# Performance work log

Hardware: AMD Instinct MI355X
Metric: run time of the kernel (lower is better)

The kernel has to match this reference:

```python
import jax, jax.numpy as jnp
import numpy as np

B, L, D = 16, 1024, 256
H, FF = 8, 2048
DH = D // H
EPS = 1e-5


def setup_inputs() -> dict:
    key = jax.random.key(0)
    ks = jax.random.split(key, 13)
    s = 0.02
    return {
        "x": jax.random.normal(ks[0], (B, L, D), jnp.float32),
        "Wq": jax.random.normal(ks[1], (D, D), jnp.float32) * s,
        "bq": jnp.zeros((D,), jnp.float32),
        "Wk": jax.random.normal(ks[2], (D, D), jnp.float32) * s,
        "bk": jnp.zeros((D,), jnp.float32),
        "Wv": jax.random.normal(ks[3], (D, D), jnp.float32) * s,
        "bv": jnp.zeros((D,), jnp.float32),
        "Wo": jax.random.normal(ks[4], (D, D), jnp.float32) * s,
        "bo": jnp.zeros((D,), jnp.float32),
        "W1": jax.random.normal(ks[5], (D, FF), jnp.float32) * s,
        "b1": jnp.zeros((FF,), jnp.float32),
        "W2": jax.random.normal(ks[6], (FF, D), jnp.float32) * s,
        "b2": jnp.zeros((D,), jnp.float32),
        "g1": jnp.ones((D,), jnp.float32),
        "be1": jnp.zeros((D,), jnp.float32),
        "g2": jnp.ones((D,), jnp.float32),
        "be2": jnp.zeros((D,), jnp.float32),
    }


def _layernorm(x, g, b):
    m = jnp.mean(x, axis=-1, keepdims=True)
    v = jnp.mean(jnp.square(x - m), axis=-1, keepdims=True)
    return (x - m) * jax.lax.rsqrt(v + EPS) * g + b


def reference(x, Wq, bq, Wk, bk, Wv, bv, Wo, bo, W1, b1, W2, b2, g1, be1, g2, be2):
    b, l, d = x.shape
    # QKV projections, split heads (torch split/cat == reshape to [b,l,H,dh])
    q = (x @ Wq + bq).reshape(b, l, H, DH)
    k = (x @ Wk + bk).reshape(b, l, H, DH)
    v = (x @ Wv + bv).reshape(b, l, H, DH)
    # scaled dot-product attention per head
    scores = jnp.einsum("bqhd,bkhd->bhqk", q, k) / np.float32(DH) ** 0.5
    attn = jax.nn.softmax(scores, axis=-1)
    o = jnp.einsum("bhqk,bkhd->bqhd", attn, v).reshape(b, l, d)
    o = o @ Wo + bo
    # residual + LN1 (dropout p=0.0 -> identity)
    h = _layernorm(x + o, g1, be1)
    # FFN + residual + LN2
    ff = jax.nn.relu(h @ W1 + b1) @ W2 + b2
    return _layernorm(h + ff, g2, be2)
```

## Files before the change

kernel.cpp:

```cpp
#include <hip/hip_runtime.h>
#include <math.h>

#define B_  16
#define L_  1024
#define D_  256
#define H_  8
#define DH_ 32
#define FF_ 2048
#define NROW (B_*L_)
#define QKVS 768

typedef __attribute__((ext_vector_type(8))) short short8;
typedef __attribute__((ext_vector_type(4))) short short4v;
typedef __attribute__((ext_vector_type(4))) float f32x4;
typedef __attribute__((ext_vector_type(4))) unsigned uint4v;
typedef __attribute__((ext_vector_type(4))) unsigned short ushort4v;
typedef unsigned short ushortT;

__device__ inline ushortT f2bf(float f) {
    unsigned u = __builtin_bit_cast(unsigned, f);
    u += 0x7fffu + ((u >> 16) & 1u);
    return (ushortT)(u >> 16);
}

__device__ inline float bf2f(ushortT u) {
    return __builtin_bit_cast(float, (unsigned)u << 16);
}

__device__ inline float fexp2(float x) {
#if __has_builtin(__builtin_amdgcn_exp2f)
    return __builtin_amdgcn_exp2f(x);
#else
    return exp2f(x);
#endif
}

__device__ inline void gload_lds16(const ushortT* g, ushortT* l) {
    __builtin_amdgcn_global_load_lds(
        (const __attribute__((address_space(1))) unsigned*)g,
        (__attribute__((address_space(3))) unsigned*)l, 16, 0, 0);
}

__device__ inline unsigned lds_addr(const void* p) {
    return (unsigned)(size_t)(const __attribute__((address_space(3))) void*)p;
}

template<bool RELU, bool OBF16>
__global__ __launch_bounds__(256)
void gemm_bf16_kernel(const ushortT* __restrict__ A, const ushortT* __restrict__ Bt,
                      const float* __restrict__ bias, void* __restrict__ Cv,
                      int K, int ldb, int ldc)
{
    __shared__ ushortT As[2][128 * 32];
    __shared__ ushortT Bs[2][128 * 32];

    const int tid   = threadIdx.x;
    const int w     = tid >> 6;
    const int lane  = tid & 63;
    const int qlane = lane & 15;
    const int g     = lane >> 4;
    const int wm    = w >> 1, wn = w & 1;
    const int m0    = (blockIdx.x & 127) * 128;
    const int n0    = (blockIdx.x >> 7) * 128;

    int srowA[2], sq[2];
    #pragma unroll
    for (int j = 0; j < 2; ++j) {
        int idx = (j * 4 + w) * 64 + lane;
        srowA[j] = idx >> 2;
        sq[j]    = (idx & 3) ^ (srowA[j] & 3);
    }
    const int rsw = (g ^ (qlane & 3)) * 8;

    f32x4 acc[4][4];
    #pragma unroll
    for (int mi = 0; mi < 4; ++mi)
        #pragma unroll
        for (int ni = 0; ni < 4; ++ni)
            acc[mi][ni] = (f32x4){0.f, 0.f, 0.f, 0.f};

    auto stage = [&](int buf, int kt) {
        const int k0 = kt * 32;
        #pragma unroll
        for (int j = 0; j < 2; ++j) {
            gload_lds16(A + (size_t)(m0 + srowA[j]) * K + k0 + sq[j] * 8,
                        &As[buf][(j * 4 + w) * 512]);
            gload_lds16(Bt + (size_t)(n0 + srowA[j]) * ldb + k0 + sq[j] * 8,
                        &Bs[buf][(j * 4 + w) * 512]);
        }
    };

    stage(0, 0);
    __syncthreads();

    const int nt = K >> 5;
    for (int t = 0; t < nt; ++t) {
        const int cur = t & 1;
        if (t + 1 < nt) stage(cur ^ 1, t + 1);

        short8 af[4], bfr[4];
        #pragma unroll
        for (int mi = 0; mi < 4; ++mi)
            af[mi] = *(const short8*)&As[cur][(wm * 64 + mi * 16 + qlane) * 32 + rsw];
        #pragma unroll
        for (int ni = 0; ni < 4; ++ni)
            bfr[ni] = *(const short8*)&Bs[cur][(wn * 64 + ni * 16 + qlane) * 32 + rsw];

        #pragma unroll
        for (int mi = 0; mi < 4; ++mi)
            #pragma unroll
            for (int ni = 0; ni < 4; ++ni)
                acc[mi][ni] = __builtin_amdgcn_mfma_f32_16x16x32_bf16(
                    af[mi], bfr[ni], acc[mi][ni], 0, 0, 0);

        __syncthreads();
    }

    #pragma unroll
    for (int mi = 0; mi < 4; ++mi) {
        #pragma unroll
        for (int ni = 0; ni < 4; ++ni) {
            const int n = n0 + wn * 64 + ni * 16 + qlane;
            const float bval = bias ? bias[n] : 0.f;
            #pragma unroll
            for (int r = 0; r < 4; ++r) {
                const int m = m0 + wm * 64 + mi * 16 + 4 * g + r;
                float v = acc[mi][ni][r] + bval;
                if (RELU)  v = fmaxf(v, 0.f);
                if (OBF16) ((ushortT*)Cv)[(size_t)m * ldc + n] = f2bf(v);
                else       ((float*)Cv)[(size_t)m * ldc + n] = v;
            }
        }
    }
}

template<bool RELU, bool OBF16>
__global__ __launch_bounds__(256)
void gemm64_kernel(const ushortT* __restrict__ A, const ushortT* __restrict__ Bt,
                   const float* __restrict__ bias, void* __restrict__ Cv,
                   int K, int ldc)
{
    __shared__ ushortT As[2][64 * 64];
    __shared__ ushortT Bs[2][64 * 64];

    const int tid   = threadIdx.x;
    const int w     = tid >> 6;
    const int lane  = tid & 63;
    const int qlane = lane & 15;
    const int g     = lane >> 4;
    const int bid   = blockIdx.x;
    const int m0    = (bid & 255) * 64;
    const int n0    = (bid >> 8) * 64;

    int srow[2], sq[2];
    #pragma unroll
    for (int j = 0; j < 2; ++j) {
        const int c = j * 256 + tid;
        srow[j] = c >> 3;
        sq[j]   = (c & 7) ^ (srow[j] & 7);
    }

    f32x4 acc[4];
    #pragma unroll
    for (int ni = 0; ni < 4; ++ni) acc[ni] = (f32x4){0.f, 0.f, 0.f, 0.f};

    auto stage = [&](int buf, int kt) {
        const int k0 = kt * 64;
        #pragma unroll
        for (int j = 0; j < 2; ++j) {
            gload_lds16(A + (size_t)(m0 + srow[j]) * K + k0 + sq[j] * 8,
                        &As[buf][(j * 256 + tid) * 8]);
            gload_lds16(Bt + (size_t)(n0 + srow[j]) * K + k0 + sq[j] * 8,
                        &Bs[buf][(j * 256 + tid) * 8]);
        }
    };

    stage(0, 0);
    __syncthreads();

    const int arow = w * 16 + qlane;
    const int nt = K >> 6;
    for (int t = 0; t < nt; ++t) {
        const int cur = t & 1;
        if (t + 1 < nt) stage(cur ^ 1, t + 1);

        #pragma unroll
        for (int ks = 0; ks < 2; ++ks) {
            const int aq = (ks * 4 + g) ^ (arow & 7);
            short8 af = *(const short8*)&As[cur][arow * 64 + aq * 8];
            #pragma unroll
            for (int ni = 0; ni < 4; ++ni) {
                const int brow = ni * 16 + qlane;
                const int bq = (ks * 4 + g) ^ (brow & 7);
                short8 bfr = *(const short8*)&Bs[cur][brow * 64 + bq * 8];
                acc[ni] = __builtin_amdgcn_mfma_f32_16x16x32_bf16(af, bfr, acc[ni], 0, 0, 0);
            }
        }

        __syncthreads();
    }

    #pragma unroll
    for (int ni = 0; ni < 4; ++ni) {
        const int n = n0 + ni * 16 + qlane;
        const float bval = bias[n];
        #pragma unroll
        for (int r = 0; r < 4; ++r) {
            const int m = m0 + w * 16 + 4 * g + r;
            float v = acc[ni][r] + bval;
            if (RELU)  v = fmaxf(v, 0.f);
            if (OBF16) ((ushortT*)Cv)[(size_t)m * ldc + n] = f2bf(v);
            else       ((float*)Cv)[(size_t)m * ldc + n] = v;
        }
    }
}

template<bool XF32, bool YF32, bool OBF16>
__global__ __launch_bounds__(256)
void ln_kernel(const void* __restrict__ X, const void* __restrict__ Y,
               const float* __restrict__ g, const float* __restrict__ bb,
               void* __restrict__ out)
{
    const int tid  = threadIdx.x;
    const int lane = tid & 63;
    const int w    = tid >> 6;
    const size_t row = (size_t)blockIdx.x * 4 + w;
    const int c    = lane * 4;

    float xv[4], yv[4];
    if (XF32) {
        float4 v = *reinterpret_cast<const float4*>((const float*)X + row * D_ + c);
        xv[0] = v.x; xv[1] = v.y; xv[2] = v.z; xv[3] = v.w;
    } else {
        ushort4v v = *reinterpret_cast<const ushort4v*>((const ushortT*)X + row * D_ + c);
        #pragma unroll
        for (int j = 0; j < 4; ++j) xv[j] = bf2f(v[j]);
    }
    if (YF32) {
        float4 v = *reinterpret_cast<const float4*>((const float*)Y + row * D_ + c);
        yv[0] = v.x; yv[1] = v.y; yv[2] = v.z; yv[3] = v.w;
    } else {
        ushort4v v = *reinterpret_cast<const ushort4v*>((const ushortT*)Y + row * D_ + c);
        #pragma unroll
        for (int j = 0; j < 4; ++j) yv[j] = bf2f(v[j]);
    }

    float s0 = xv[0] + yv[0], s1 = xv[1] + yv[1], s2 = xv[2] + yv[2], s3 = xv[3] + yv[3];

    float sum = s0 + s1 + s2 + s3;
    float sq  = s0 * s0 + s1 * s1 + s2 * s2 + s3 * s3;
    #pragma unroll
    for (int off = 1; off < 64; off <<= 1) {
        sum += __shfl_xor(sum, off);
        sq  += __shfl_xor(sq, off);
    }
    const float mean = sum * (1.f / D_);
    const float var  = sq * (1.f / D_) - mean * mean;
    const float rinv = rsqrtf(var + 1e-5f);

    const float4 gv = *reinterpret_cast<const float4*>(g + c);
    const float4 bv = *reinterpret_cast<const float4*>(bb + c);
    float o0 = (s0 - mean) * rinv * gv.x + bv.x;
    float o1 = (s1 - mean) * rinv * gv.y + bv.y;
    float o2 = (s2 - mean) * rinv * gv.z + bv.z;
    float o3 = (s3 - mean) * rinv * gv.w + bv.w;

    if (OBF16) {
        unsigned p0 = (unsigned)f2bf(o0) | ((unsigned)f2bf(o1) << 16);
        unsigned p1 = (unsigned)f2bf(o2) | ((unsigned)f2bf(o3) << 16);
        uint2 u = {p0, p1};
        *reinterpret_cast<uint2*>((ushortT*)out + row * D_ + c) = u;
    } else {
        float4 ov = {o0, o1, o2, o3};
        *reinterpret_cast<float4*>((float*)out + row * D_ + c) = ov;
    }
}

__global__ __launch_bounds__(512)
void attn_mfma_kernel(const ushortT* __restrict__ qkv, ushortT* __restrict__ o)
{
    __shared__ __align__(16) ushortT K4[2][2][2048];
    __shared__ __align__(16) ushortT Vs[2][2][2048];

    const int tid   = threadIdx.x;
    const int lane  = tid & 63;
    const int w     = tid >> 6;
    const int qlane = lane & 15;
    const int g     = lane >> 4;

    const int bid = blockIdx.x;
    const int bh  = bid & 127;
    const int b   = bh >> 3;
    const int h   = bh & 7;
    const int q0  = (bid >> 7) * 128;

    const size_t inbase = (size_t)b * L_ * QKVS + h * 32;
    const size_t obase  = (size_t)b * L_ * 256 + h * 32;

    const short8 qf = *(const short8*)(qkv + inbase + (size_t)(q0 + w * 16 + qlane) * QKVS + g * 8);

    f32x4 ot0 = {0.f, 0.f, 0.f, 0.f}, ot1 = {0.f, 0.f, 0.f, 0.f};
    float l_reg = 0.f;

    const float CEXP = 0.25503540f;

    const int t2   = tid & 255;
    const int skey = t2 >> 2;
    const int sg   = t2 & 3;
    const bool isK = tid < 256;
    const ushortT* src = qkv + inbase + (isK ? 256 : 512) + sg * 8 + (size_t)skey * QKVS;

    char* K4b = (char*)&K4[0][0][0];
    char* Vsb = (char*)&Vs[0][0][0];

    unsigned kwoff = (unsigned)sg * 1024u + (unsigned)skey * 16u;
    kwoff ^= (kwoff >> 5) & 0x60;
    const unsigned vwoff = ((unsigned)((skey >> 2) * 2 + (sg >> 1))) * 128u +
                           ((unsigned)(skey & 3)) * 32u +
                           ((((unsigned)(sg & 1)) ^ ((unsigned)(sg >> 1))) * 16u);
    char* wbase = isK ? K4b : Vsb;
    const unsigned woff = isK ? kwoff : vwoff;

    unsigned kroff[4];
    #pragma unroll
    for (int kt4 = 0; kt4 < 4; ++kt4) {
        unsigned off = (unsigned)g * 1024u + (unsigned)(kt4 * 16 + qlane) * 16u;
        kroff[kt4] = off ^ ((off >> 5) & 0x60);
    }
    const unsigned vrbase  = lds_addr(&Vs[0][0][0]) + 256u * (unsigned)g + 8u * (unsigned)qlane;
    const unsigned vrbase2 = vrbase ^ 64u;

    short8 reg0 = *(const short8*)src;
    short8 reg1 = *(const short8*)(src + (size_t)64 * QKVS);

    for (int t = 0; t < L_ / 128; ++t) {
        const unsigned bo = (unsigned)(t & 1) * 8192u;
        *(short8*)(wbase + bo + woff)         = reg0;
        *(short8*)(wbase + bo + 4096u + woff) = reg1;
        if (t + 1 < L_ / 128) {
            const size_t roff = (size_t)((t + 1) * 128) * QKVS;
            reg0 = *(const short8*)(src + roff);
            reg1 = *(const short8*)(src + roff + (size_t)64 * QKVS);
        }
        __syncthreads();

        #pragma unroll
        for (int sub = 0; sub < 2; ++sub) {
            const unsigned so = bo + (unsigned)sub * 4096u;

            f32x4 st[4];
            __builtin_amdgcn_s_setprio(1);
            #pragma unroll
            for (int kt4 = 0; kt4 < 4; ++kt4) {
                short8 kf = *(const short8*)(K4b + so + kroff[kt4]);
                st[kt4] = __builtin_amdgcn_mfma_f32_16x16x32_bf16(kf, qf, (f32x4){0.f,0.f,0.f,0.f}, 0, 0, 0);
            }
            __builtin_amdgcn_s_setprio(0);

            float p[16];
            float s4[4];
            #pragma unroll
            for (int kt4 = 0; kt4 < 4; ++kt4) {
                #pragma unroll
                for (int r = 0; r < 4; ++r)
                    p[kt4 * 4 + r] = fexp2(st[kt4][r] * CEXP);
                s4[kt4] = (p[kt4*4] + p[kt4*4+1]) + (p[kt4*4+2] + p[kt4*4+3]);
            }
            float ssum = (s4[0] + s4[1]) + (s4[2] + s4[3]);
            ssum += __shfl_xor(ssum, 16);
            ssum += __shfl_xor(ssum, 32);
            l_reg += ssum;

            unsigned pk_[8];
            #pragma unroll
            for (int i = 0; i < 8; ++i)
                asm("v_cvt_pk_bf16_f32 %0, %1, %2" : "=v"(pk_[i]) : "v"(p[2*i]), "v"(p[2*i+1]));
            const short8 pa0 = __builtin_bit_cast(short8, (uint4v){pk_[0], pk_[1], pk_[2], pk_[3]});
            const short8 pa1 = __builtin_bit_cast(short8, (uint4v){pk_[4], pk_[5], pk_[6], pk_[7]});

            const unsigned va  = vrbase  + so;
            const unsigned va2 = vrbase2 + so;
            __builtin_amdgcn_s_setprio(1);
            {
                short4v v00, v01, v10, v11;
                asm volatile("ds_read_b64_tr_b16 %0, %1"             : "=v"(v00) : "v"(va));
                asm volatile("ds_read_b64_tr_b16 %0, %1 offset:1024" : "=v"(v01) : "v"(va));
                asm volatile("ds_read_b64_tr_b16 %0, %1 offset:128"  : "=v"(v10) : "v"(va2));
                asm volatile("ds_read_b64_tr_b16 %0, %1 offset:1152" : "=v"(v11) : "v"(va2));
                asm volatile("s_waitcnt lgkmcnt(0)" ::: "memory");
                __builtin_amdgcn_sched_barrier(0);
                short8 vb0 = __builtin_shufflevector(v00, v01, 0,1,2,3,4,5,6,7);
                short8 vb1 = __builtin_shufflevector(v10, v11, 0,1,2,3,4,5,6,7);
                ot0 = __builtin_amdgcn_mfma_f32_16x16x32_bf16(pa0, vb0, ot0, 0, 0, 0);
                ot1 = __builtin_amdgcn_mfma_f32_16x16x32_bf16(pa0, vb1, ot1, 0, 0, 0);
            }
            {
                short4v v00, v01, v10, v11;
                asm volatile("ds_read_b64_tr_b16 %0, %1 offset:2048" : "=v"(v00) : "v"(va));
                asm volatile("ds_read_b64_tr_b16 %0, %1 offset:3072" : "=v"(v01) : "v"(va));
                asm volatile("ds_read_b64_tr_b16 %0, %1 offset:2176" : "=v"(v10) : "v"(va2));
                asm volatile("ds_read_b64_tr_b16 %0, %1 offset:3200" : "=v"(v11) : "v"(va2));
                asm volatile("s_waitcnt lgkmcnt(0)" ::: "memory");
                __builtin_amdgcn_sched_barrier(0);
                short8 vb0 = __builtin_shufflevector(v00, v01, 0,1,2,3,4,5,6,7);
                short8 vb1 = __builtin_shufflevector(v10, v11, 0,1,2,3,4,5,6,7);
                ot0 = __builtin_amdgcn_mfma_f32_16x16x32_bf16(pa1, vb0, ot0, 0, 0, 0);
                ot1 = __builtin_amdgcn_mfma_f32_16x16x32_bf16(pa1, vb1, ot1, 0, 0, 0);
            }
            __builtin_amdgcn_s_setprio(0);
        }
    }

    const float linv = 1.f / l_reg;
    #pragma unroll
    for (int r = 0; r < 4; ++r) {
        float lr = __shfl(linv, 4 * g + r);
        size_t row = (size_t)(q0 + w * 16 + 4 * g + r);
        ushortT* op = o + obase + row * 256;
        op[qlane]      = f2bf(ot0[r] * lr);
        op[16 + qlane] = f2bf(ot1[r] * lr);
    }
}

__global__ __launch_bounds__(256)
void prep_kernel(const float* __restrict__ x, ushortT* __restrict__ xb,
                 const float* __restrict__ Wq, const float* __restrict__ Wk,
                 const float* __restrict__ Wv, const float* __restrict__ Wo,
                 ushortT* __restrict__ Wqkvb, ushortT* __restrict__ Wob,
                 const float* __restrict__ W1, ushortT* __restrict__ W1b,
                 const float* __restrict__ W2, ushortT* __restrict__ W2b,
                 const float* __restrict__ bq, const float* __restrict__ bk,
                 const float* __restrict__ bv, float* __restrict__ bqkv)
{
    __shared__ float t[32][33];
    const int bid = blockIdx.x;
    const int tid = threadIdx.x;

    if (bid < 4096) {
        const int i = (bid * 256 + tid) * 4;
        float4 v = *reinterpret_cast<const float4*>(x + i);
        unsigned p0 = (unsigned)f2bf(v.x) | ((unsigned)f2bf(v.y) << 16);
        unsigned p1 = (unsigned)f2bf(v.z) | ((unsigned)f2bf(v.w) << 16);
        uint2 u = {p0, p1};
        *reinterpret_cast<uint2*>(xb + i) = u;
        return;
    }
    int i = bid - 4096;
    const float* W; ushortT* Wt; int K, N, bx, by;
    if (i < 256) {
        const int which = i >> 6, j = i & 63;
        bx = j & 7; by = j >> 3; K = 256; N = 256;
        W  = which == 0 ? Wq : which == 1 ? Wk : which == 2 ? Wv : Wo;
        Wt = which == 0 ? Wqkvb : which == 1 ? Wqkvb + 65536
           : which == 2 ? Wqkvb + 131072 : Wob;
    } else if (i < 768) {
        const int j = i - 256; bx = j & 63; by = j >> 6; K = 256; N = 2048;
        W = W1; Wt = W1b;
    } else if (i < 1280) {
        const int j = i - 768; bx = j & 7; by = j >> 3; K = 2048; N = 256;
        W = W2; Wt = W2b;
    } else {
        for (int k = tid; k < 768; k += 256)
            bqkv[k] = k < 256 ? bq[k] : (k < 512 ? bk[k - 256] : bv[k - 512]);
        return;
    }
    const int tx = tid & 31, ty = tid >> 5;
    const int k0 = by * 32, n0 = bx * 32;
    #pragma unroll
    for (int r = ty; r < 32; r += 8) t[r][tx] = W[(size_t)(k0 + r) * N + n0 + tx];
    __syncthreads();
    #pragma unroll
    for (int r = ty; r < 32; r += 8) Wt[(size_t)(n0 + r) * K + k0 + tx] = f2bf(t[tx][r]);
}

extern "C" void kernel_launch(void* const* d_in, const int* in_sizes, int n_in,
                              void* d_out, int out_size, void* d_ws, size_t ws_size,
                              hipStream_t stream)
{
    const float* x   = (const float*)d_in[0];
    const float* Wq  = (const float*)d_in[1];
    const float* bq  = (const float*)d_in[2];
    const float* Wk  = (const float*)d_in[3];
    const float* bk  = (const float*)d_in[4];
    const float* Wv  = (const float*)d_in[5];
    const float* bv  = (const float*)d_in[6];
    const float* Wo  = (const float*)d_in[7];
    const float* bo  = (const float*)d_in[8];
    const float* W1  = (const float*)d_in[9];
    const float* b1  = (const float*)d_in[10];
    const float* W2  = (const float*)d_in[11];
    const float* b2  = (const float*)d_in[12];
    const float* g1  = (const float*)d_in[13];
    const float* be1 = (const float*)d_in[14];
    const float* g2  = (const float*)d_in[15];
    const float* be2 = (const float*)d_in[16];
    float* out = (float*)d_out;

    char* wsb = (char*)d_ws;
    const size_t MB = (size_t)1 << 20;
    ushortT* Wqkvb = (ushortT*)(wsb);
    ushortT* Wob   = (ushortT*)(wsb + 393216);
    ushortT* W1b   = (ushortT*)(wsb + 512 * 1024);
    ushortT* W2b   = (ushortT*)(wsb + 1536 * 1024);
    float*   bqkv  = (float*)  (wsb + 2560 * 1024);
    ushortT* xb  = (ushortT*)(wsb + 3 * MB);
    ushortT* qkv = (ushortT*)(wsb + 11 * MB);
    ushortT* ob  = (ushortT*)(wsb + 35 * MB);
    ushortT* ao  = (ushortT*)(wsb + 43 * MB);
    ushortT* hb  = (ushortT*)(wsb + 3 * MB);
    ushortT* f1  = (ushortT*)(wsb + 11 * MB);

    prep_kernel<<<dim3(5377), dim3(256), 0, stream>>>(
        x, xb, Wq, Wk, Wv, Wo, Wqkvb, Wob, W1, W1b, W2, W2b, bq, bk, bv, bqkv);

    gemm_bf16_kernel<false, true><<<dim3(768), dim3(256), 0, stream>>>(
        xb, Wqkvb, bqkv, qkv, 256, 256, QKVS);

    attn_mfma_kernel<<<dim3(1024), dim3(512), 0, stream>>>(qkv, ob);

    gemm64_kernel<false, true><<<dim3(1024), dim3(256), 0, stream>>>(
        ob, Wob, bo, ao, 256, 256);

    ln_kernel<false, false, true><<<dim3(NROW / 4), dim3(256), 0, stream>>>(
        xb, ao, g1, be1, hb);

    gemm64_kernel<true, true><<<dim3(8192), dim3(256), 0, stream>>>(
        hb, W1b, b1, f1, 256, FF_);

    gemm64_kernel<false, false><<<dim3(1024), dim3(256), 0, stream>>>(
        f1, W2b, b2, out, 2048, 256);

    ln_kernel<false, true, false><<<dim3(NROW / 4), dim3(256), 0, stream>>>(
        hb, out, g2, be2, out);
}
```

Baseline: 137.9 us.

## Pack FFN1 outputs with permuted columns and shrink attention K/V tile

The FFN1 GEMM epilogue now writes four bias-added, ReLU'd bf16 values per lane as one packed 8-byte store, using hardware bf16 pack conversion. The columns of the intermediate activation are permuted to make this possible, and the prep kernel permutes W2's K dimension to match so the FFN2 result is unchanged. This replaces scalar 2-byte scattered stores on the largest intermediate tensor. Separately, the attention kernel stages 64 keys per iteration instead of 128, halving shared memory, which may raise occupancy at the cost of twice as many barriers.

```diff
diff --git a/kernel.cpp b/kernel.cpp
--- a/kernel.cpp
+++ b/kernel.cpp
@@ -134,7 +134,7 @@
     }
 }
 
-template<bool RELU, bool OBF16>
+template<bool RELU, bool OBF16, bool PACKPERM>
 __global__ __launch_bounds__(256)
 void gemm64_kernel(const ushortT* __restrict__ A, const ushortT* __restrict__ Bt,
                    const float* __restrict__ bias, void* __restrict__ Cv,
@@ -200,17 +200,38 @@
         __syncthreads();
     }
 
-    #pragma unroll
-    for (int ni = 0; ni < 4; ++ni) {
-        const int n = n0 + ni * 16 + qlane;
-        const float bval = bias[n];
+    if (PACKPERM) {
+        float bval[4];
+        #pragma unroll
+        for (int ni = 0; ni < 4; ++ni) bval[ni] = bias[n0 + ni * 16 + qlane];
         #pragma unroll
         for (int r = 0; r < 4; ++r) {
             const int m = m0 + w * 16 + 4 * g + r;
-            float v = acc[ni][r] + bval;
-            if (RELU)  v = fmaxf(v, 0.f);
-            if (OBF16) ((ushortT*)Cv)[(size_t)m * ldc + n] = f2bf(v);
-            else       ((float*)Cv)[(size_t)m * ldc + n] = v;
+            float v0 = acc[0][r] + bval[0], v1 = acc[1][r] + bval[1];
+            float v2 = acc[2][r] + bval[2], v3 = acc[3][r] + bval[3];
+            if (RELU) {
+                v0 = fmaxf(v0, 0.f); v1 = fmaxf(v1, 0.f);
+                v2 = fmaxf(v2, 0.f); v3 = fmaxf(v3, 0.f);
+            }
+            unsigned lo, hi;
+            asm("v_cvt_pk_bf16_f32 %0, %1, %2" : "=v"(lo) : "v"(v0), "v"(v1));
+            asm("v_cvt_pk_bf16_f32 %0, %1, %2" : "=v"(hi) : "v"(v2), "v"(v3));
+            uint2 u = {lo, hi};
+            *reinterpret_cast<uint2*>(&((ushortT*)Cv)[(size_t)m * ldc + n0 + qlane * 4]) = u;
+        }
+    } else {
+        #pragma unroll
+        for (int ni = 0; ni < 4; ++ni) {
+            const int n = n0 + ni * 16 + qlane;
+            const float bval = bias[n];
+            #pragma unroll
+            for (int r = 0; r < 4; ++r) {
+                const int m = m0 + w * 16 + 4 * g + r;
+                float v = acc[ni][r] + bval;
+                if (RELU)  v = fmaxf(v, 0.f);
+                if (OBF16) ((ushortT*)Cv)[(size_t)m * ldc + n] = f2bf(v);
+                else       ((float*)Cv)[(size_t)m * ldc + n] = v;
+            }
         }
     }
 }
@@ -279,8 +300,8 @@
 __global__ __launch_bounds__(512)
 void attn_mfma_kernel(const ushortT* __restrict__ qkv, ushortT* __restrict__ o)
 {
-    __shared__ __align__(16) ushortT K4[2][2][2048];
-    __shared__ __align__(16) ushortT Vs[2][2][2048];
+    __shared__ __align__(16) ushortT K4[2][2048];
+    __shared__ __align__(16) ushortT Vs[2][2048];
 
     const int tid   = threadIdx.x;
     const int lane  = tid & 63;
@@ -310,8 +331,8 @@
     const bool isK = tid < 256;
     const ushortT* src = qkv + inbase + (isK ? 256 : 512) + sg * 8 + (size_t)skey * QKVS;
 
-    char* K4b = (char*)&K4[0][0][0];
-    char* Vsb = (char*)&Vs[0][0][0];
+    char* K4b = (char*)&K4[0][0];
+    char* Vsb = (char*)&Vs[0][0];
 
     unsigned kwoff = (unsigned)sg * 1024u + (unsigned)skey * 16u;
     kwoff ^= (kwoff >> 5) & 0x60;
@@ -327,88 +348,79 @@
         unsigned off = (unsigned)g * 1024u + (unsigned)(kt4 * 16 + qlane) * 16u;
         kroff[kt4] = off ^ ((off >> 5) & 0x60);
     }
-    const unsigned vrbase  = lds_addr(&Vs[0][0][0]) + 256u * (unsigned)g + 8u * (unsigned)qlane;
+    const unsigned vrbase  = lds_addr(&Vs[0][0]) + 256u * (unsigned)g + 8u * (unsigned)qlane;
     const unsigned vrbase2 = vrbase ^ 64u;
 
-    short8 reg0 = *(const short8*)src;
-    short8 reg1 = *(const short8*)(src + (size_t)64 * QKVS);
-
-    for (int t = 0; t < L_ / 128; ++t) {
-        const unsigned bo = (unsigned)(t & 1) * 8192u;
-        *(short8*)(wbase + bo + woff)         = reg0;
-        *(short8*)(wbase + bo + 4096u + woff) = reg1;
-        if (t + 1 < L_ / 128) {
-            const size_t roff = (size_t)((t + 1) * 128) * QKVS;
-            reg0 = *(const short8*)(src + roff);
-            reg1 = *(const short8*)(src + roff + (size_t)64 * QKVS);
-        }
+    short8 reg = *(const short8*)src;
+
+    #pragma unroll 2
+    for (int t = 0; t < L_ / 64; ++t) {
+        const unsigned bo = (unsigned)(t & 1) * 4096u;
+        *(short8*)(wbase + bo + woff) = reg;
+        if (t + 1 < L_ / 64)
+            reg = *(const short8*)(src + (size_t)((t + 1) * 64) * QKVS);
         __syncthreads();
 
-        #pragma unroll
-        for (int sub = 0; sub < 2; ++sub) {
-            const unsigned so = bo + (unsigned)sub * 4096u;
-
-            f32x4 st[4];
-            __builtin_amdgcn_s_setprio(1);
+        f32x4 st[4];
+        __builtin_amdgcn_s_setprio(1);
+        #pragma unroll
+        for (int kt4 = 0; kt4 < 4; ++kt4) {
+            short8 kf = *(const short8*)(K4b + bo + kroff[kt4]);
+            st[kt4] = __builtin_amdgcn_mfma_f32_16x16x32_bf16(kf, qf, (f32x4){0.f,0.f,0.f,0.f}, 0, 0, 0);
+        }
+        __builtin_amdgcn_s_setprio(0);
+
+        float p[16];
+        float s4[4];
+        #pragma unroll
+        for (int kt4 = 0; kt4 < 4; ++kt4) {
             #pragma unroll
-            for (int kt4 = 0; kt4 < 4; ++kt4) {
-                short8 kf = *(const short8*)(K4b + so + kroff[kt4]);
-                st[kt4] = __builtin_amdgcn_mfma_f32_16x16x32_bf16(kf, qf, (f32x4){0.f,0.f,0.f,0.f}, 0, 0, 0);
-            }
-            __builtin_amdgcn_s_setprio(0);
-
-            float p[16];
-            float s4[4];
-            #pragma unroll
-            for (int kt4 = 0; kt4 < 4; ++kt4) {
-                #pragma unroll
-                for (int r = 0; r < 4; ++r)
-                    p[kt4 * 4 + r] = fexp2(st[kt4][r] * CEXP);
-                s4[kt4] = (p[kt4*4] + p[kt4*4+1]) + (p[kt4*4+2] + p[kt4*4+3]);
-            }
-            float ssum = (s4[0] + s4[1]) + (s4[2] + s4[3]);
-            ssum += __shfl_xor(ssum, 16);
-            ssum += __shfl_xor(ssum, 32);
-            l_reg += ssum;
-
-            unsigned pk_[8];
-            #pragma unroll
-            for (int i = 0; i < 8; ++i)
-                asm("v_cvt_pk_bf16_f32 %0, %1, %2" : "=v"(pk_[i]) : "v"(p[2*i]), "v"(p[2*i+1]));
-            const short8 pa0 = __builtin_bit_cast(short8, (uint4v){pk_[0], pk_[1], pk_[2], pk_[3]});
-            const short8 pa1 = __builtin_bit_cast(short8, (uint4v){pk_[4], pk_[5], pk_[6], pk_[7]});
-
-            const unsigned va  = vrbase  + so;
-            const unsigned va2 = vrbase2 + so;
-            __builtin_amdgcn_s_setprio(1);
-            {
-                short4v v00, v01, v10, v11;
-                asm volatile("ds_read_b64_tr_b16 %0, %1"             : "=v"(v00) : "v"(va));
-                asm volatile("ds_read_b64_tr_b16 %0, %1 offset:1024" : "=v"(v01) : "v"(va));
-                asm volatile("ds_read_b64_tr_b16 %0, %1 offset:128"  : "=v"(v10) : "v"(va2));
-                asm volatile("ds_read_b64_tr_b16 %0, %1 offset:1152" : "=v"(v11) : "v"(va2));
-                asm volatile("s_waitcnt lgkmcnt(0)" ::: "memory");
-                __builtin_amdgcn_sched_barrier(0);
-                short8 vb0 = __builtin_shufflevector(v00, v01, 0,1,2,3,4,5,6,7);
-                short8 vb1 = __builtin_shufflevector(v10, v11, 0,1,2,3,4,5,6,7);
-                ot0 = __builtin_amdgcn_mfma_f32_16x16x32_bf16(pa0, vb0, ot0, 0, 0, 0);
-                ot1 = __builtin_amdgcn_mfma_f32_16x16x32_bf16(pa0, vb1, ot1, 0, 0, 0);
-            }
-            {
-                short4v v00, v01, v10, v11;
-                asm volatile("ds_read_b64_tr_b16 %0, %1 offset:2048" : "=v"(v00) : "v"(va));
-                asm volatile("ds_read_b64_tr_b16 %0, %1 offset:3072" : "=v"(v01) : "v"(va));
-                asm volatile("ds_read_b64_tr_b16 %0, %1 offset:2176" : "=v"(v10) : "v"(va2));
-                asm volatile("ds_read_b64_tr_b16 %0, %1 offset:3200" : "=v"(v11) : "v"(va2));
-                asm volatile("s_waitcnt lgkmcnt(0)" ::: "memory");
-                __builtin_amdgcn_sched_barrier(0);
-                short8 vb0 = __builtin_shufflevector(v00, v01, 0,1,2,3,4,5,6,7);
-                short8 vb1 = __builtin_shufflevector(v10, v11, 0,1,2,3,4,5,6,7);
-                ot0 = __builtin_amdgcn_mfma_f32_16x16x32_bf16(pa1, vb0, ot0, 0, 0, 0);
-                ot1 = __builtin_amdgcn_mfma_f32_16x16x32_bf16(pa1, vb1, ot1, 0, 0, 0);
-            }
-            __builtin_amdgcn_s_setprio(0);
-        }
+            for (int r = 0; r < 4; ++r)
+                p[kt4 * 4 + r] = fexp2(st[kt4][r] * CEXP);
+            s4[kt4] = (p[kt4*4] + p[kt4*4+1]) + (p[kt4*4+2] + p[kt4*4+3]);
+        }
+        float ssum = (s4[0] + s4[1]) + (s4[2] + s4[3]);
+        ssum += __shfl_xor(ssum, 16);
+        ssum += __shfl_xor(ssum, 32);
+        l_reg += ssum;
+
+        unsigned pk_[8];
+        #pragma unroll
+        for (int i = 0; i < 8; ++i)
+            asm("v_cvt_pk_bf16_f32 %0, %1, %2" : "=v"(pk_[i]) : "v"(p[2*i]), "v"(p[2*i+1]));
+        const short8 pa0 = __builtin_bit_cast(short8, (uint4v){pk_[0], pk_[1], pk_[2], pk_[3]});
+        const short8 pa1 = __builtin_bit_cast(short8, (uint4v){pk_[4], pk_[5], pk_[6], pk_[7]});
+
+        const unsigned va  = vrbase  + bo;
+        const unsigned va2 = vrbase2 + bo;
+        __builtin_amdgcn_s_setprio(1);
+        {
+            short4v v00, v01, v10, v11;
+            asm volatile("ds_read_b64_tr_b16 %0, %1"             : "=v"(v00) : "v"(va));
+            asm volatile("ds_read_b64_tr_b16 %0, %1 offset:1024" : "=v"(v01) : "v"(va));
+            asm volatile("ds_read_b64_tr_b16 %0, %1 offset:128"  : "=v"(v10) : "v"(va2));
+            asm volatile("ds_read_b64_tr_b16 %0, %1 offset:1152" : "=v"(v11) : "v"(va2));
+            asm volatile("s_waitcnt lgkmcnt(0)" ::: "memory");
+            __builtin_amdgcn_sched_barrier(0);
+            short8 vb0 = __builtin_shufflevector(v00, v01, 0,1,2,3,4,5,6,7);
+            short8 vb1 = __builtin_shufflevector(v10, v11, 0,1,2,3,4,5,6,7);
+            ot0 = __builtin_amdgcn_mfma_f32_16x16x32_bf16(pa0, vb0, ot0, 0, 0, 0);
+            ot1 = __builtin_amdgcn_mfma_f32_16x16x32_bf16(pa0, vb1, ot1, 0, 0, 0);
+        }
+        {
+            short4v v00, v01, v10, v11;
+            asm volatile("ds_read_b64_tr_b16 %0, %1 offset:2048" : "=v"(v00) : "v"(va));
+            asm volatile("ds_read_b64_tr_b16 %0, %1 offset:3072" : "=v"(v01) : "v"(va));
+            asm volatile("ds_read_b64_tr_b16 %0, %1 offset:2176" : "=v"(v10) : "v"(va2));
+            asm volatile("ds_read_b64_tr_b16 %0, %1 offset:3200" : "=v"(v11) : "v"(va2));
+            asm volatile("s_waitcnt lgkmcnt(0)" ::: "memory");
+            __builtin_amdgcn_sched_barrier(0);
+            short8 vb0 = __builtin_shufflevector(v00, v01, 0,1,2,3,4,5,6,7);
+            short8 vb1 = __builtin_shufflevector(v10, v11, 0,1,2,3,4,5,6,7);
+            ot0 = __builtin_amdgcn_mfma_f32_16x16x32_bf16(pa1, vb0, ot0, 0, 0, 0);
+            ot1 = __builtin_amdgcn_mfma_f32_16x16x32_bf16(pa1, vb1, ot1, 0, 0, 0);
+        }
+        __builtin_amdgcn_s_setprio(0);
     }
 
     const float linv = 1.f / l_reg;
@@ -446,7 +458,7 @@
         return;
     }
     int i = bid - 4096;
-    const float* W; ushortT* Wt; int K, N, bx, by;
+    const float* W; ushortT* Wt; int K, N, bx, by; bool permk = false;
     if (i < 256) {
         const int which = i >> 6, j = i & 63;
         bx = j & 7; by = j >> 3; K = 256; N = 256;
@@ -458,7 +470,7 @@
         W = W1; Wt = W1b;
     } else if (i < 1280) {
         const int j = i - 768; bx = j & 7; by = j >> 3; K = 2048; N = 256;
-        W = W2; Wt = W2b;
+        W = W2; Wt = W2b; permk = true;
     } else {
         for (int k = tid; k < 768; k += 256)
             bqkv[k] = k < 256 ? bq[k] : (k < 512 ? bk[k - 256] : bv[k - 512]);
@@ -470,7 +482,11 @@
     for (int r = ty; r < 32; r += 8) t[r][tx] = W[(size_t)(k0 + r) * N + n0 + tx];
     __syncthreads();
     #pragma unroll
-    for (int r = ty; r < 32; r += 8) Wt[(size_t)(n0 + r) * K + k0 + tx] = f2bf(t[tx][r]);
+    for (int r = ty; r < 32; r += 8) {
+        int k = k0 + tx;
+        if (permk) k = (k & ~63) | ((k & 15) * 4) | ((k >> 4) & 3);
+        Wt[(size_t)(n0 + r) * K + k] = f2bf(t[tx][r]);
+    }
 }
 
 extern "C" void kernel_launch(void* const* d_in, const int* in_sizes, int n_in,
@@ -518,16 +534,16 @@
 
     attn_mfma_kernel<<<dim3(1024), dim3(512), 0, stream>>>(qkv, ob);
 
-    gemm64_kernel<false, true><<<dim3(1024), dim3(256), 0, stream>>>(
+    gemm64_kernel<false, true, false><<<dim3(1024), dim3(256), 0, stream>>>(
         ob, Wob, bo, ao, 256, 256);
 
     ln_kernel<false, false, true><<<dim3(NROW / 4), dim3(256), 0, stream>>>(
         xb, ao, g1, be1, hb);
 
-    gemm64_kernel<true, true><<<dim3(8192), dim3(256), 0, stream>>>(
+    gemm64_kernel<true, true, true><<<dim3(8192), dim3(256), 0, stream>>>(
         hb, W1b, b1, f1, 256, FF_);
 
-    gemm64_kernel<false, false><<<dim3(1024), dim3(256), 0, stream>>>(
+    gemm64_kernel<false, false, false><<<dim3(1024), dim3(256), 0, stream>>>(
         f1, W2b, b2, out, 2048, 256);
 
     ln_kernel<false, true, false><<<dim3(NROW / 4), dim3(256), 0, stream>>>(
```

Measured after the change: 134.3 us. -2.6%, faster.
